# Optimization experiments

Hardware: AMD Instinct MI355X
Metric: run time of the kernel (lower is better)

Reference implementation:

```python
import jax, jax.numpy as jnp
import numpy as np

DN = ('NCHW', 'OIHW', 'NCHW')

def bn(x, g, b, m, v, eps=1e-5):
    # inference-mode BatchNorm2d over channel dim of NCHW
    s = g * jax.lax.rsqrt(v + eps)
    return x * s[:, None, None] + (b - m * s)[:, None, None]

def conv2d(x, w, pad):
    return jax.lax.conv_general_dilated(x, w, (1, 1), pad, dimension_numbers=DN)

def mamba(x, in_w, cw, cb, xp_w, dt_w, dt_b, A_log, Dp, out_w):
    # x: [B, L, d_model]
    B, L, dm = x.shape
    di = cw.shape[0]           # d_inner
    N = A_log.shape[1]         # d_state
    R = dt_w.shape[1]          # dt_rank
    K = cw.shape[2]            # d_conv
    xz = x @ in_w.T            # [B, L, 2*di]
    xi, z = xz[..., :di], xz[..., di:]
    # causal depthwise conv1d along L
    xc = jnp.transpose(xi, (0, 2, 1))  # [B, di, L]
    xc = jax.lax.conv_general_dilated(xc, cw, (1,), [(K - 1, 0)],
                                      dimension_numbers=('NCH', 'OIH', 'NCH'),
                                      feature_group_count=di)
    xc = jax.nn.silu(xc + cb[None, :, None])
    xc = jnp.transpose(xc, (0, 2, 1))  # [B, L, di]
    dbl = xc @ xp_w.T                  # [B, L, R+2N]
    dt, Bs, Cs = dbl[..., :R], dbl[..., R:R + N], dbl[..., R + N:]
    dt = jax.nn.softplus(dt @ dt_w.T + dt_b)        # [B, L, di]
    A = -jnp.exp(A_log)                              # [di, N]
    dA = jnp.exp(dt[..., None] * A)                  # [B, L, di, N]
    dBx = dt[..., None] * Bs[:, :, None, :] * xc[..., None]  # [B, L, di, N]

    def step(h, inp):
        a, bx, c = inp                               # [B,di,N],[B,di,N],[B,N]
        h = a * h + bx
        return h, jnp.einsum('bdn,bn->bd', h, c)

    h0 = jnp.zeros((B, di, N), x.dtype)
    _, ys = jax.lax.scan(step, h0, (jnp.transpose(dA, (1, 0, 2, 3)),
                                    jnp.transpose(dBx, (1, 0, 2, 3)),
                                    jnp.transpose(Cs, (1, 0, 2))))
    y = jnp.transpose(ys, (1, 0, 2)) + xc * Dp       # skip via D
    y = y * jax.nn.silu(z)                           # gate
    return y @ out_w.T                               # [B, L, dm]

def fwd(x, w1, g1, b1, m1, v1, w2, g2, b2, m2, v2,
        in_w, cw, cb, xp_w, dt_w, dt_b, A_log, Dp, out_w,
        w3, g3, b3, m3, v3, w4, g4, b4, m4, v4):
    x = jax.nn.gelu(bn(conv2d(x, w1, [(1, 1), (1, 1)]), g1, b1, m1, v1), approximate=False)
    x = jax.nn.silu(bn(conv2d(x, w2, [(0, 0), (0, 0)]), g2, b2, m2, v2))
    Bsz, Dc, H, W = x.shape
    t = jnp.transpose(x, (0, 2, 3, 1)).reshape(Bsz, H * W, Dc)
    t = mamba(t, in_w, cw, cb, xp_w, dt_w, dt_b, A_log, Dp, out_w)
    x = jnp.transpose(t.reshape(Bsz, H, W, Dc), (0, 3, 1, 2))
    x = jax.nn.silu(bn(conv2d(x, w3, [(0, 0), (0, 0)]), g3, b3, m3, v3))
    x = jax.nn.gelu(bn(conv2d(x, w4, [(1, 1), (1, 1)]), g4, b4, m4, v4), approximate=False)
    return x

def setup_inputs() -> dict:
    INC, D, OUTC = 96, 192, 192
    DI, N, R, K = 2 * D, 16, 12, 4   # d_inner, d_state, dt_rank, d_conv
    B, H, W = 8, 32, 32
    ks = jax.random.split(jax.random.key(0), 32)
    rn = lambda i, sh, s=0.05: s * jax.random.normal(ks[i], sh, dtype=jnp.float32)
    def bnp(i, c):
        k1, k2, k3, k4 = jax.random.split(ks[i], 4)
        return (1.0 + 0.1 * jax.random.normal(k1, (c,), dtype=jnp.float32),
                0.1 * jax.random.normal(k2, (c,), dtype=jnp.float32),
                0.1 * jax.random.normal(k3, (c,), dtype=jnp.float32),
                jax.random.uniform(k4, (c,), jnp.float32, 0.5, 1.5))
    g1, b1, m1, v1 = bnp(2, INC)
    g2, b2, m2, v2 = bnp(4, D)
    g3, b3, m3, v3 = bnp(6, OUTC)
    g4, b4, m4, v4 = bnp(8, OUTC)
    A_log = jnp.log(jnp.broadcast_to(jnp.arange(1, N + 1, dtype=jnp.float32), (DI, N)))
    return {
        'x': jax.random.normal(ks[0], (B, INC, H, W), dtype=jnp.float32),
        'w1': rn(1, (INC, INC, 3, 3)), 'g1': g1, 'b1': b1, 'm1': m1, 'v1': v1,
        'w2': rn(3, (D, INC, 1, 1)), 'g2': g2, 'b2': b2, 'm2': m2, 'v2': v2,
        'in_w': rn(10, (2 * DI, D), 0.02),
        'cw': rn(11, (DI, 1, K), 0.2),
        'cb': rn(12, (DI,), 0.02),
        'xp_w': rn(13, (R + 2 * N, DI), 0.05),
        'dt_w': rn(14, (DI, R), 0.1),
        'dt_b': rn(15, (DI,), 0.1) - 4.0,
        'A_log': A_log,
        'Dp': jnp.ones((DI,), dtype=jnp.float32),
        'out_w': rn(16, (D, DI), 0.05),
        'w3': rn(5, (OUTC, D, 1, 1)), 'g3': g3, 'b3': b3, 'm3': m3, 'v3': v3,
        'w4': rn(7, (OUTC, OUTC, 3, 3), 0.03), 'g4': g4, 'b4': b4, 'm4': m4, 'v4': v4,
    }

def reference(x, w1, g1, b1, m1, v1, w2, g2, b2, m2, v2,
              in_w, cw, cb, xp_w, dt_w, dt_b, A_log, Dp, out_w,
              w3, g3, b3, m3, v3, w4, g4, b4, m4, v4):
    return fwd(x, w1, g1, b1, m1, v1, w2, g2, b2, m2, v2,
               in_w, cw, cb, xp_w, dt_w, dt_b, A_log, Dp, out_w,
               w3, g3, b3, m3, v3, w4, g4, b4, m4, v4)
```

## Files before the change

### kernel.cpp

```cpp
#include <hip/hip_runtime.h>
#include <hip/hip_bf16.h>

using u16 = unsigned short;
using short8 = __attribute__((ext_vector_type(8))) short;
using f32x4  = __attribute__((ext_vector_type(4))) float;

constexpr int DI_ = 384;

constexpr size_t O_XZ   = 0;
constexpr size_t O_XCT  = O_XZ  + (size_t)8192*384;
constexpr size_t O_ZST  = O_XCT + (size_t)384*8192;
constexpr size_t O_DBLT = O_ZST + (size_t)384*8192;
constexpr size_t O_YFT  = O_DBLT+ (size_t)32*8192;
constexpr size_t O_B16  = O_YFT + (size_t)384*8192;
constexpr size_t O_DTT  = O_XZ;
constexpr size_t B_T1  = 0;
constexpr size_t B_T2  = B_T1  + (size_t)8192*96;
constexpr size_t B_XC  = B_T2  + (size_t)8192*192;
constexpr size_t B_XB1 = B_XC  + (size_t)8192*384;
constexpr size_t B_XB4 = B_XB1 + (size_t)8192*96;
constexpr size_t B_WT1 = B_XB4 + (size_t)8192*192;
constexpr size_t B_WT4 = B_WT1 + (size_t)9*96*96;
constexpr size_t B_INW = B_WT4 + (size_t)9*192*192;
constexpr size_t B_W2  = B_INW + (size_t)768*192;
constexpr size_t B_XP  = B_W2  + (size_t)192*96;
constexpr size_t B_WDT = B_XP  + (size_t)32*384;
constexpr size_t B_WOW = B_WDT + (size_t)384*384;

__device__ __forceinline__ u16 f2b(float f) {
    __hip_bfloat16 h = __float2bfloat16(f);
    return *reinterpret_cast<u16*>(&h);
}

struct PrepArgs {
    const float *w1, *w4, *in_w, *w2, *xp_w, *dt_w, *w3, *out_w, *x;
    u16 *wt1, *wt4, *inwb, *w2b, *xpb, *Wdt, *Wow, *Xb1;
};

__global__ __launch_bounds__(256) void prep_k(PrepArgs a) {
    const int job = blockIdx.y;
    const int stride = gridDim.x * 256;
    const int i0 = blockIdx.x * 256 + threadIdx.x;
    switch (job) {
    case 0:
        for (int i = i0; i < 9*96*96; i += stride) {
            int ci = i % 96, co = (i / 96) % 96, t = i / (96*96);
            a.wt1[i] = f2b(a.w1[((size_t)co*96 + ci)*9 + t]);
        } break;
    case 1:
        for (int i = i0; i < 9*192*192; i += stride) {
            int ci = i % 192, co = (i / 192) % 192, t = i / (192*192);
            a.wt4[i] = f2b(a.w4[((size_t)co*192 + ci)*9 + t]);
        } break;
    case 2:
        for (int i = i0; i < 768*192; i += stride) a.inwb[i] = f2b(a.in_w[i]);
        break;
    case 3:
        for (int i = i0; i < 192*96; i += stride) a.w2b[i] = f2b(a.w2[i]);
        break;
    case 4:
        for (int i = i0; i < 32*384; i += stride) {
            int r = i / 384, c = i % 384;
            a.xpb[i] = f2b(a.xp_w[(size_t)(12 + r)*384 + c]);
        } break;
    case 5:
        for (int i = i0; i < 384*384; i += stride) {
            int r = i / 384, c = i % 384;
            float s = 0.f;
            #pragma unroll
            for (int k = 0; k < 12; ++k) s += a.dt_w[r*12 + k] * a.xp_w[(size_t)k*384 + c];
            a.Wdt[i] = f2b(s);
        } break;
    case 6:
        for (int i = i0; i < 192*384; i += stride) {
            int o = i / 384, d = i % 384;
            float s = 0.f;
            for (int j = 0; j < 192; ++j) s += a.w3[(size_t)o*192 + j] * a.out_w[(size_t)j*384 + d];
            a.Wow[i] = f2b(s);
        } break;
    case 7:
        for (int i = i0; i < 8192*96; i += stride) {
            int ci = i % 96, px = i / 96;
            a.Xb1[i] = f2b(a.x[(((size_t)(px >> 10) * 96 + ci) << 10) | (size_t)(px & 1023)]);
        } break;
    }
}

template<int CIN, int COUT, int NTILE, int OUTM>
__global__ __launch_bounds__(256) void conv3x3_mfma_k(
    const u16* __restrict__ Xb, const u16* __restrict__ Wt,
    const float* __restrict__ g, const float* __restrict__ b,
    const float* __restrict__ m, const float* __restrict__ v,
    void* __restrict__ out)
{
    constexpr int LD = 40;
    constexpr int NT = NTILE / 16;
    __shared__ u16 As[4 * 36 * LD];
    __shared__ u16 Bs[9 * NTILE * LD];
    const int tid = threadIdx.x;
    const int wave = tid >> 6, lane = tid & 63;
    const int quad = lane >> 4, l16 = lane & 15;
    const int rowBase = blockIdx.x * 64;
    const int colBase = blockIdx.y * NTILE;
    const int img = rowBase >> 10;
    const int imgRow0 = (rowBase & 1023) >> 5;

    if (tid < 160) {
        int slot8 = tid / 20;
        int off = tid % 20;
        int hrow = slot8 >> 1;
        int hcol = (slot8 & 1) ? 33 : 0;
        ((unsigned*)As)[((hrow * 36 + hcol) * LD) / 2 + off] = 0u;
    }

    f32x4 acc[NT];
    #pragma unroll
    for (int nt = 0; nt < NT; ++nt)
        #pragma unroll
        for (int i = 0; i < 4; ++i) acc[nt][i] = 0.f;

    const int pxl = wave * 16 + l16;
    const int prow = pxl >> 5, pcol = pxl & 31;

    for (int ci0 = 0; ci0 < CIN; ci0 += 32) {
        __syncthreads();
        #pragma unroll
        for (int it = 0; it < 2; ++it) {
            int id = tid + it * 256;
            int pix = id >> 2, seg = id & 3;
            int hrow = pix >> 5, hcol = pix & 31;
            int grow = imgRow0 - 1 + hrow;
            uint4 va = make_uint4(0u, 0u, 0u, 0u);
            if ((unsigned)grow < 32u)
                va = *(const uint4*)(Xb +
                    (size_t)((img << 10) + (grow << 5) + hcol) * CIN + ci0 + seg * 8);
            *(uint4*)(As + (hrow * 36 + hcol + 1) * LD + seg * 8) = va;
        }
        constexpr int BT = 9 * NTILE * 4;
        for (int id = tid; id < BT; id += 256) {
            int t = id / (NTILE * 4);
            int r = (id >> 2) & (NTILE - 1);
            int seg = id & 3;
            uint4 vb = *(const uint4*)(Wt +
                ((size_t)t * COUT + colBase + r) * CIN + ci0 + seg * 8);
            *(uint4*)(Bs + (t * NTILE + r) * LD + seg * 8) = vb;
        }
        __syncthreads();
        #pragma unroll
        for (int t = 0; t < 9; ++t) {
            const int dr = t / 3 - 1, dc = t % 3 - 1;
            short8 a = *(const short8*)(As +
                ((prow + 1 + dr) * 36 + (pcol + 1 + dc)) * LD + quad * 8);
            #pragma unroll
            for (int nt = 0; nt < NT; ++nt) {
                short8 bf = *(const short8*)(Bs + (t * NTILE + nt * 16 + l16) * LD + quad * 8);
                acc[nt] = __builtin_amdgcn_mfma_f32_16x16x32_bf16(a, bf, acc[nt], 0, 0, 0);
            }
        }
    }

    const int px0 = rowBase + wave * 16 + quad * 4;
    #pragma unroll
    for (int nt = 0; nt < NT; ++nt) {
        const int co = colBase + nt * 16 + l16;
        const float sc = g[co] * rsqrtf(v[co] + 1e-5f);
        const float bb = b[co] - m[co] * sc;
        float o[4];
        #pragma unroll
        for (int r = 0; r < 4; ++r) {
            float xv = acc[nt][r] * sc + bb;
            o[r] = 0.5f * xv * (1.f + erff(xv * 0.70710678f));
        }
        if (OUTM == 2) {
            #pragma unroll
            for (int r = 0; r < 4; ++r)
                ((u16*)out)[(size_t)(px0 + r) * COUT + co] = f2b(o[r]);
        } else {
            const int oimg = px0 >> 10, off = px0 & 1023;
            *(float4*)((float*)out + (((size_t)oimg * COUT + co) << 10) + off) =
                make_float4(o[0], o[1], o[2], o[3]);
        }
    }
}

template<int NTILE, int EPI, int OUTM>
__device__ __forceinline__ void gemm_body(
    int M, int N, int K,
    const u16* __restrict__ Ab, const u16* __restrict__ Bb, void* __restrict__ C,
    const float* __restrict__ p0, const float* __restrict__ p1,
    const float* __restrict__ p2, const float* __restrict__ p3,
    int rowBase, int colBase, u16* As, u16* Bs)
{
    constexpr int LDA = 40;
    constexpr int NT = NTILE / 16;
    const int tid = threadIdx.x;
    const int wave = tid >> 6, lane = tid & 63;
    const int quad = lane >> 4, l16 = lane & 15;

    f32x4 acc[NT];
    #pragma unroll
    for (int nt = 0; nt < NT; ++nt)
        #pragma unroll
        for (int i = 0; i < 4; ++i) acc[nt][i] = 0.f;

    const int ar = tid >> 2, aseg = tid & 3;

    for (int k0 = 0; k0 < K; k0 += 32) {
        __syncthreads();
        uint4 va = *(const uint4*)(Ab + (size_t)(rowBase + ar) * K + k0 + aseg * 8);
        *(uint4*)(As + ar * LDA + aseg * 8) = va;
        if (tid < NTILE * 4) {
            int r = tid >> 2, seg = tid & 3;
            uint4 vb = *(const uint4*)(Bb + (size_t)(colBase + r) * K + k0 + seg * 8);
            *(uint4*)(Bs + r * LDA + seg * 8) = vb;
        }
        __syncthreads();
        short8 a = *(const short8*)(As + (wave * 16 + l16) * LDA + quad * 8);
        #pragma unroll
        for (int nt = 0; nt < NT; ++nt) {
            short8 bf = *(const short8*)(Bs + (nt * 16 + l16) * LDA + quad * 8);
            acc[nt] = __builtin_amdgcn_mfma_f32_16x16x32_bf16(a, bf, acc[nt], 0, 0, 0);
        }
    }

    const int px0 = rowBase + wave * 16 + quad * 4;
    #pragma unroll
    for (int nt = 0; nt < NT; ++nt) {
        const int co = colBase + nt * 16 + l16;
        float sc = 0.f, bb = 0.f;
        if (EPI == 1) {
            sc = p0[co] * rsqrtf(p3[co] + 1e-5f);
            bb = p1[co] - p2[co] * sc;
        } else if (EPI == 2) {
            bb = p0[co];
        }
        float o[4];
        #pragma unroll
        for (int r = 0; r < 4; ++r) {
            float xv = acc[nt][r];
            if (EPI == 1) {
                xv = xv * sc + bb;
                xv = xv / (1.f + __expf(-xv));
            } else if (EPI == 2) {
                xv += bb;
                xv = (xv > 20.f) ? xv : log1pf(__expf(xv));
            } else if (EPI == 3) {
                xv = xv / (1.f + __expf(-xv));
            }
            o[r] = xv;
        }
        if (OUTM == 3) {
            *(float4*)((float*)C + (size_t)co * M + px0) =
                make_float4(o[0], o[1], o[2], o[3]);
        } else if (OUTM == 2) {
            #pragma unroll
            for (int r = 0; r < 4; ++r)
                ((u16*)C)[(size_t)(px0 + r) * N + co] = f2b(o[r]);
        } else {
            #pragma unroll
            for (int r = 0; r < 4; ++r)
                ((float*)C)[(size_t)(px0 + r) * N + co] = o[r];
        }
    }
}

template<int NTILE, int EPI, int OUTM>
__global__ __launch_bounds__(256) void gemm_mfma_k(
    int M, int N, int K,
    const u16* __restrict__ Ab, const u16* __restrict__ Bb, void* __restrict__ C,
    const float* __restrict__ p0, const float* __restrict__ p1,
    const float* __restrict__ p2, const float* __restrict__ p3)
{
    __shared__ u16 As[64 * 40];
    __shared__ u16 Bs[NTILE * 40];
    gemm_body<NTILE, EPI, OUTM>(M, N, K, Ab, Bb, C, p0, p1, p2, p3,
                                blockIdx.x * 64, blockIdx.y * NTILE, As, Bs);
}

__global__ __launch_bounds__(256) void ip_k(
    const u16* __restrict__ t2b, const u16* __restrict__ inwb,
    float* __restrict__ xzb, float* __restrict__ zst)
{
    __shared__ u16 As[64 * 40];
    __shared__ u16 Bs[64 * 40];
    if (blockIdx.y < 6) {
        gemm_body<64, 0, 0>(8192, 384, 192, t2b, inwb, xzb,
                            nullptr, nullptr, nullptr, nullptr,
                            blockIdx.x * 64, blockIdx.y * 64, As, Bs);
    } else {
        gemm_body<64, 3, 3>(8192, 384, 192, t2b, inwb + (size_t)384*192, zst,
                            nullptr, nullptr, nullptr, nullptr,
                            blockIdx.x * 64, (blockIdx.y - 6) * 64, As, Bs);
    }
}

__global__ __launch_bounds__(256) void pd_k(
    const u16* __restrict__ xcb, const u16* __restrict__ Wdt,
    const u16* __restrict__ xpb, const float* __restrict__ dt_b,
    float* __restrict__ dtt, float* __restrict__ dblt)
{
    __shared__ u16 As[64 * 40];
    __shared__ u16 Bs[64 * 40];
    if (blockIdx.y < 6) {
        gemm_body<64, 2, 3>(8192, 384, 384, xcb, Wdt, dtt, dt_b, nullptr, nullptr, nullptr,
                            blockIdx.x * 64, blockIdx.y * 64, As, Bs);
    } else {
        gemm_body<32, 0, 3>(8192, 32, 384, xcb, xpb, dblt, nullptr, nullptr, nullptr, nullptr,
                            blockIdx.x * 64, 0, As, Bs);
    }
}

__global__ __launch_bounds__(256) void gemm_at_k(
    int M, int N, int K,
    const float* __restrict__ At, const u16* __restrict__ Bb, u16* __restrict__ C,
    const float* __restrict__ p0, const float* __restrict__ p1,
    const float* __restrict__ p2, const float* __restrict__ p3)
{
    constexpr int LDA = 40;
    constexpr int NTILE = 64, NT = 4;
    __shared__ u16 As[64 * LDA];
    __shared__ u16 Bs[NTILE * LDA];
    const int tid = threadIdx.x;
    const int wave = tid >> 6, lane = tid & 63;
    const int quad = lane >> 4, l16 = lane & 15;
    const int rowBase = blockIdx.x * 64;
    const int colBase = blockIdx.y * NTILE;

    f32x4 acc[NT];
    #pragma unroll
    for (int nt = 0; nt < NT; ++nt)
        #pragma unroll
        for (int i = 0; i < 4; ++i) acc[nt][i] = 0.f;

    const int krow = tid >> 3, mseg = tid & 7;

    for (int k0 = 0; k0 < K; k0 += 32) {
        __syncthreads();
        const float* src = At + (size_t)(k0 + krow) * M + rowBase + mseg * 4;
        float4 f0 = *(const float4*)(src);
        float4 f1 = *(const float4*)(src + 32);
        As[(mseg*4 + 0) * LDA + krow] = f2b(f0.x);
        As[(mseg*4 + 1) * LDA + krow] = f2b(f0.y);
        As[(mseg*4 + 2) * LDA + krow] = f2b(f0.z);
        As[(mseg*4 + 3) * LDA + krow] = f2b(f0.w);
        As[(mseg*4 + 32) * LDA + krow] = f2b(f1.x);
        As[(mseg*4 + 33) * LDA + krow] = f2b(f1.y);
        As[(mseg*4 + 34) * LDA + krow] = f2b(f1.z);
        As[(mseg*4 + 35) * LDA + krow] = f2b(f1.w);
        if (tid < NTILE * 4) {
            int r = tid >> 2, seg = tid & 3;
            uint4 vb = *(const uint4*)(Bb + (size_t)(colBase + r) * K + k0 + seg * 8);
            *(uint4*)(Bs + r * LDA + seg * 8) = vb;
        }
        __syncthreads();
        short8 a = *(const short8*)(As + (wave * 16 + l16) * LDA + quad * 8);
        #pragma unroll
        for (int nt = 0; nt < NT; ++nt) {
            short8 bf = *(const short8*)(Bs + (nt * 16 + l16) * LDA + quad * 8);
            acc[nt] = __builtin_amdgcn_mfma_f32_16x16x32_bf16(a, bf, acc[nt], 0, 0, 0);
        }
    }

    const int px0 = rowBase + wave * 16 + quad * 4;
    #pragma unroll
    for (int nt = 0; nt < NT; ++nt) {
        const int co = colBase + nt * 16 + l16;
        const float sc = p0[co] * rsqrtf(p3[co] + 1e-5f);
        const float bb = p1[co] - p2[co] * sc;
        #pragma unroll
        for (int r = 0; r < 4; ++r) {
            float xv = acc[nt][r] * sc + bb;
            xv = xv / (1.f + __expf(-xv));
            C[(size_t)(px0 + r) * N + co] = f2b(xv);
        }
    }
}

__global__ __launch_bounds__(256) void dwconv_k(
    const float* __restrict__ xz, const float* __restrict__ cw, const float* __restrict__ cb,
    u16* __restrict__ xcb, float* __restrict__ xct)
{
    __shared__ float T[64][65];
    const int tid = threadIdx.x;
    const int cl = tid & 63, rq = tid >> 6;
    const int mBase = blockIdx.x * 64, cBase = blockIdx.y * 64;
    const int c = cBase + cl;
    const float w0 = cw[c*4+0], w1 = cw[c*4+1], w2 = cw[c*4+2], w3 = cw[c*4+3];
    const float bias = cb[c];
    #pragma unroll
    for (int rr = 0; rr < 16; ++rr) {
        int ml = rr * 4 + rq;
        int bl = mBase + ml;
        int l = bl & 1023;
        float acc = bias + xz[(size_t)bl * 384 + c] * w3;
        if (l >= 1) acc += xz[(size_t)(bl-1) * 384 + c] * w2;
        if (l >= 2) acc += xz[(size_t)(bl-2) * 384 + c] * w1;
        if (l >= 3) acc += xz[(size_t)(bl-3) * 384 + c] * w0;
        float s = acc / (1.f + __expf(-acc));
        xcb[(size_t)bl * DI_ + c] = f2b(s);
        T[ml][cl] = s;
    }
    __syncthreads();
    #pragma unroll
    for (int rr = 0; rr < 16; ++rr) {
        int dl = rr * 4 + rq;
        xct[(size_t)(cBase + dl) * 8192 + mBase + cl] = T[cl][dl];
    }
}

__global__ __launch_bounds__(256) void scan_k(
    const float* __restrict__ dtt, const float* __restrict__ dblt,
    const float* __restrict__ xct, const float* __restrict__ zst,
    const float* __restrict__ A_log, const float* __restrict__ Dp,
    float* __restrict__ yft)
{
    const int bd = blockIdx.x;
    const int b = bd / DI_, d = bd % DI_;
    const int tid = threadIdx.x;
    const size_t tb = (size_t)d * 8192 + (size_t)b * 1024;
    const size_t nb = (size_t)b * 1024;
    const int t4 = tid * 4;

    __shared__ float LH[16][257];
    __shared__ float SD[257];
    __shared__ float SH[16][17];
    __shared__ float SP[16][17];
    __shared__ float SSD[17];
    __shared__ float AndS[16];

    const float4 dt4 = *(const float4*)(dtt + tb + t4);
    const float4 xc4 = *(const float4*)(xct + tb + t4);
    const float dtxc[4] = {dt4.x*xc4.x, dt4.y*xc4.y, dt4.z*xc4.z, dt4.w*xc4.w};

    float And[16];
    #pragma unroll
    for (int n = 0; n < 16; ++n) And[n] = -__expf(A_log[d*16 + n]);
    if (tid < 16) AndS[tid] = -__expf(A_log[d*16 + tid]);
    SD[tid] = dt4.x + dt4.y + dt4.z + dt4.w;

    #pragma unroll
    for (int n = 0; n < 16; ++n) {
        const float4 bs4 = *(const float4*)(dblt + (size_t)n * 8192 + nb + t4);
        float h = dtxc[0] * bs4.x;
        h = __expf(dt4.y * And[n]) * h + dtxc[1] * bs4.y;
        h = __expf(dt4.z * And[n]) * h + dtxc[2] * bs4.z;
        h = __expf(dt4.w * And[n]) * h + dtxc[3] * bs4.w;
        LH[n][tid] = h;
    }
    __syncthreads();

    {
        const int n = tid & 15, s = tid >> 4;
        const float An = AndS[n];
        float H = 0.f, ssd = 0.f;
        #pragma unroll
        for (int k = 0; k < 16; ++k) {
            const int c = s * 16 + k;
            float sd = SD[c];
            H = __expf(An * sd) * H + LH[n][c];
            ssd += sd;
        }
        SH[n][s] = H;
        if (n == 0) SSD[s] = ssd;
    }
    __syncthreads();

    if (tid < 16) {
        const float An = AndS[tid];
        float Hp = 0.f;
        #pragma unroll
        for (int s = 0; s < 16; ++s) {
            SP[tid][s] = Hp;
            Hp = __expf(An * SSD[s]) * Hp + SH[tid][s];
        }
    }
    __syncthreads();

    {
        const int n = tid & 15, s = tid >> 4;
        const float An = AndS[n];
        float st = SP[n][s];
        #pragma unroll
        for (int k = 0; k < 16; ++k) {
            const int c = s * 16 + k;
            float a = __expf(An * SD[c]);
            float h = LH[n][c];
            LH[n][c] = st;
            st = a * st + h;
        }
    }
    __syncthreads();

    float y0 = 0.f, y1 = 0.f, y2 = 0.f, y3 = 0.f;
    #pragma unroll
    for (int n = 0; n < 16; ++n) {
        float h = LH[n][tid];
        const float4 bs4 = *(const float4*)(dblt + (size_t)n * 8192 + nb + t4);
        const float4 cs4 = *(const float4*)(dblt + (size_t)(16 + n) * 8192 + nb + t4);
        h = __expf(dt4.x * And[n]) * h + dtxc[0]*bs4.x; y0 += h * cs4.x;
        h = __expf(dt4.y * And[n]) * h + dtxc[1]*bs4.y; y1 += h * cs4.y;
        h = __expf(dt4.z * And[n]) * h + dtxc[2]*bs4.z; y2 += h * cs4.z;
        h = __expf(dt4.w * And[n]) * h + dtxc[3]*bs4.w; y3 += h * cs4.w;
    }
    const float dp = Dp[d];
    const float4 zs4 = *(const float4*)(zst + tb + t4);
    float4 o;
    o.x = (y0 + xc4.x * dp) * zs4.x;
    o.y = (y1 + xc4.y * dp) * zs4.y;
    o.z = (y2 + xc4.z * dp) * zs4.z;
    o.w = (y3 + xc4.w * dp) * zs4.w;
    *(float4*)(yft + tb + t4) = o;
}

extern "C" void kernel_launch(void* const* d_in, const int* in_sizes, int n_in,
                              void* d_out, int out_size, void* d_ws, size_t ws_size,
                              hipStream_t stream) {
    const float* x     = (const float*)d_in[0];
    const float* w1    = (const float*)d_in[1];
    const float* g1    = (const float*)d_in[2];
    const float* b1    = (const float*)d_in[3];
    const float* m1    = (const float*)d_in[4];
    const float* v1    = (const float*)d_in[5];
    const float* w2    = (const float*)d_in[6];
    const float* g2    = (const float*)d_in[7];
    const float* b2    = (const float*)d_in[8];
    const float* m2    = (const float*)d_in[9];
    const float* v2    = (const float*)d_in[10];
    const float* in_w  = (const float*)d_in[11];
    const float* cw    = (const float*)d_in[12];
    const float* cb    = (const float*)d_in[13];
    const float* xp_w  = (const float*)d_in[14];
    const float* dt_w  = (const float*)d_in[15];
    const float* dt_b  = (const float*)d_in[16];
    const float* A_log = (const float*)d_in[17];
    const float* Dp    = (const float*)d_in[18];
    const float* out_w = (const float*)d_in[19];
    const float* w3    = (const float*)d_in[20];
    const float* g3    = (const float*)d_in[21];
    const float* b3    = (const float*)d_in[22];
    const float* m3    = (const float*)d_in[23];
    const float* v3    = (const float*)d_in[24];
    const float* w4    = (const float*)d_in[25];
    const float* g4    = (const float*)d_in[26];
    const float* b4    = (const float*)d_in[27];
    const float* m4    = (const float*)d_in[28];
    const float* v4    = (const float*)d_in[29];

    float* ws   = (float*)d_ws;
    float* xzb  = ws + O_XZ;
    float* xct  = ws + O_XCT;
    float* zst  = ws + O_ZST;
    float* dblt = ws + O_DBLT;
    float* yft  = ws + O_YFT;
    float* dtt  = ws + O_DTT;
    u16* b16  = (u16*)(ws + O_B16);
    u16* t1b  = b16 + B_T1;
    u16* t2b  = b16 + B_T2;
    u16* xcb  = b16 + B_XC;
    u16* Xb1  = b16 + B_XB1;
    u16* Xb4  = b16 + B_XB4;
    u16* wt1  = b16 + B_WT1;
    u16* wt4  = b16 + B_WT4;
    u16* inwb = b16 + B_INW;
    u16* w2b  = b16 + B_W2;
    u16* xpb  = b16 + B_XP;
    u16* Wdt  = b16 + B_WDT;
    u16* Wow  = b16 + B_WOW;

    PrepArgs pa;
    pa.w1 = w1; pa.w4 = w4; pa.in_w = in_w; pa.w2 = w2; pa.xp_w = xp_w;
    pa.dt_w = dt_w; pa.w3 = w3; pa.out_w = out_w; pa.x = x;
    pa.wt1 = wt1; pa.wt4 = wt4; pa.inwb = inwb; pa.w2b = w2b; pa.xpb = xpb;
    pa.Wdt = Wdt; pa.Wow = Wow; pa.Xb1 = Xb1;
    prep_k<<<dim3(256, 8), 256, 0, stream>>>(pa);

    conv3x3_mfma_k<96, 96, 32, 2><<<dim3(128, 3), 256, 0, stream>>>(
        Xb1, wt1, g1, b1, m1, v1, t1b);

    gemm_mfma_k<64, 1, 2><<<dim3(128, 3), 256, 0, stream>>>(
        8192, 192, 96, t1b, w2b, t2b, g2, b2, m2, v2);

    ip_k<<<dim3(128, 12), 256, 0, stream>>>(t2b, inwb, xzb, zst);

    dwconv_k<<<dim3(128, 6), 256, 0, stream>>>(xzb, cw, cb, xcb, xct);

    pd_k<<<dim3(128, 7), 256, 0, stream>>>(xcb, Wdt, xpb, dt_b, dtt, dblt);

    scan_k<<<8 * DI_, 256, 0, stream>>>(dtt, dblt, xct, zst, A_log, Dp, yft);

    gemm_at_k<<<dim3(128, 3), 256, 0, stream>>>(
        8192, 192, 384, yft, Wow, Xb4, g3, b3, m3, v3);

    conv3x3_mfma_k<192, 192, 64, 1><<<dim3(128, 3), 256, 0, stream>>>(
        Xb4, wt4, g4, b4, m4, v4, (float*)d_out);
}
```

Before: 264.7 us.

## Store Mamba intermediates in bf16, stage conv output through LDS, retile final conv

The in-projection now writes xz and the gated z buffer as bf16 instead of fp32. The depthwise conv and scan kernels read these bf16 values and the transposed conv output as bf16, which halves the memory traffic for these intermediates. The final conv's NCHW fp32 epilogue now transposes through shared memory so each store is a coalesced float4 row. Its column tile is halved from 64 to 32, doubling the grid to add parallelism. The bf16 storage lowers the precision of the xz, z and xc values used in the scan.

```diff
diff --git a/kernel.cpp b/kernel.cpp
--- a/kernel.cpp
+++ b/kernel.cpp
@@ -31,6 +31,11 @@
     __hip_bfloat16 h = __float2bfloat16(f);
     return *reinterpret_cast<u16*>(&h);
 }
+__device__ __forceinline__ float b2f(u16 u) {
+    return __uint_as_float(((unsigned)u) << 16);
+}
+__device__ __forceinline__ float b2f_lo(unsigned u) { return __uint_as_float(u << 16); }
+__device__ __forceinline__ float b2f_hi(unsigned u) { return __uint_as_float(u & 0xffff0000u); }
 
 struct PrepArgs {
     const float *w1, *w4, *in_w, *w2, *xp_w, *dt_w, *w3, *out_w, *x;
@@ -160,25 +165,42 @@
     }
 
     const int px0 = rowBase + wave * 16 + quad * 4;
-    #pragma unroll
-    for (int nt = 0; nt < NT; ++nt) {
-        const int co = colBase + nt * 16 + l16;
-        const float sc = g[co] * rsqrtf(v[co] + 1e-5f);
-        const float bb = b[co] - m[co] * sc;
-        float o[4];
-        #pragma unroll
-        for (int r = 0; r < 4; ++r) {
-            float xv = acc[nt][r] * sc + bb;
-            o[r] = 0.5f * xv * (1.f + erff(xv * 0.70710678f));
-        }
-        if (OUTM == 2) {
+    if (OUTM == 2) {
+        #pragma unroll
+        for (int nt = 0; nt < NT; ++nt) {
+            const int co = colBase + nt * 16 + l16;
+            const float sc = g[co] * rsqrtf(v[co] + 1e-5f);
+            const float bb = b[co] - m[co] * sc;
             #pragma unroll
-            for (int r = 0; r < 4; ++r)
-                ((u16*)out)[(size_t)(px0 + r) * COUT + co] = f2b(o[r]);
-        } else {
-            const int oimg = px0 >> 10, off = px0 & 1023;
-            *(float4*)((float*)out + (((size_t)oimg * COUT + co) << 10) + off) =
-                make_float4(o[0], o[1], o[2], o[3]);
+            for (int r = 0; r < 4; ++r) {
+                float xv = acc[nt][r] * sc + bb;
+                float gel = 0.5f * xv * (1.f + erff(xv * 0.70710678f));
+                ((u16*)out)[(size_t)(px0 + r) * COUT + co] = f2b(gel);
+            }
+        }
+    } else {
+        float* Tout = (float*)As;
+        const int pxl0 = wave * 16 + quad * 4;
+        __syncthreads();
+        #pragma unroll
+        for (int nt = 0; nt < NT; ++nt) {
+            const int co = colBase + nt * 16 + l16;
+            const float sc = g[co] * rsqrtf(v[co] + 1e-5f);
+            const float bb = b[co] - m[co] * sc;
+            #pragma unroll
+            for (int r = 0; r < 4; ++r) {
+                float xv = acc[nt][r] * sc + bb;
+                Tout[(nt * 16 + l16) * 68 + pxl0 + r] =
+                    0.5f * xv * (1.f + erff(xv * 0.70710678f));
+            }
+        }
+        __syncthreads();
+        const int off0 = rowBase & 1023;
+        for (int s = tid; s < NTILE * 16; s += 256) {
+            int co = s >> 4, p4 = s & 15;
+            float4 vv = *(const float4*)(Tout + co * 68 + p4 * 4);
+            *(float4*)((float*)out + (((size_t)img * COUT + colBase + co) << 10)
+                       + off0 + p4 * 4) = vv;
         }
     }
 }
@@ -252,6 +274,11 @@
         if (OUTM == 3) {
             *(float4*)((float*)C + (size_t)co * M + px0) =
                 make_float4(o[0], o[1], o[2], o[3]);
+        } else if (OUTM == 4) {
+            uint2 pk;
+            pk.x = (unsigned)f2b(o[0]) | ((unsigned)f2b(o[1]) << 16);
+            pk.y = (unsigned)f2b(o[2]) | ((unsigned)f2b(o[3]) << 16);
+            *(uint2*)((u16*)C + (size_t)co * M + px0) = pk;
         } else if (OUTM == 2) {
             #pragma unroll
             for (int r = 0; r < 4; ++r)
@@ -279,16 +306,16 @@
 
 __global__ __launch_bounds__(256) void ip_k(
     const u16* __restrict__ t2b, const u16* __restrict__ inwb,
-    float* __restrict__ xzb, float* __restrict__ zst)
+    u16* __restrict__ xzb16, u16* __restrict__ zst16)
 {
     __shared__ u16 As[64 * 40];
     __shared__ u16 Bs[64 * 40];
     if (blockIdx.y < 6) {
-        gemm_body<64, 0, 0>(8192, 384, 192, t2b, inwb, xzb,
+        gemm_body<64, 0, 2>(8192, 384, 192, t2b, inwb, xzb16,
                             nullptr, nullptr, nullptr, nullptr,
                             blockIdx.x * 64, blockIdx.y * 64, As, Bs);
     } else {
-        gemm_body<64, 3, 3>(8192, 384, 192, t2b, inwb + (size_t)384*192, zst,
+        gemm_body<64, 3, 4>(8192, 384, 192, t2b, inwb + (size_t)384*192, zst16,
                             nullptr, nullptr, nullptr, nullptr,
                             blockIdx.x * 64, (blockIdx.y - 6) * 64, As, Bs);
     }
@@ -377,8 +404,8 @@
 }
 
 __global__ __launch_bounds__(256) void dwconv_k(
-    const float* __restrict__ xz, const float* __restrict__ cw, const float* __restrict__ cb,
-    u16* __restrict__ xcb, float* __restrict__ xct)
+    const u16* __restrict__ xz16, const float* __restrict__ cw, const float* __restrict__ cb,
+    u16* __restrict__ xcb, u16* __restrict__ xct16)
 {
     __shared__ float T[64][65];
     const int tid = threadIdx.x;
@@ -392,10 +419,10 @@
         int ml = rr * 4 + rq;
         int bl = mBase + ml;
         int l = bl & 1023;
-        float acc = bias + xz[(size_t)bl * 384 + c] * w3;
-        if (l >= 1) acc += xz[(size_t)(bl-1) * 384 + c] * w2;
-        if (l >= 2) acc += xz[(size_t)(bl-2) * 384 + c] * w1;
-        if (l >= 3) acc += xz[(size_t)(bl-3) * 384 + c] * w0;
+        float acc = bias + b2f(xz16[(size_t)bl * 384 + c]) * w3;
+        if (l >= 1) acc += b2f(xz16[(size_t)(bl-1) * 384 + c]) * w2;
+        if (l >= 2) acc += b2f(xz16[(size_t)(bl-2) * 384 + c]) * w1;
+        if (l >= 3) acc += b2f(xz16[(size_t)(bl-3) * 384 + c]) * w0;
         float s = acc / (1.f + __expf(-acc));
         xcb[(size_t)bl * DI_ + c] = f2b(s);
         T[ml][cl] = s;
@@ -404,13 +431,13 @@
     #pragma unroll
     for (int rr = 0; rr < 16; ++rr) {
         int dl = rr * 4 + rq;
-        xct[(size_t)(cBase + dl) * 8192 + mBase + cl] = T[cl][dl];
+        xct16[(size_t)(cBase + dl) * 8192 + mBase + cl] = f2b(T[cl][dl]);
     }
 }
 
 __global__ __launch_bounds__(256) void scan_k(
     const float* __restrict__ dtt, const float* __restrict__ dblt,
-    const float* __restrict__ xct, const float* __restrict__ zst,
+    const u16* __restrict__ xct16, const u16* __restrict__ zst16,
     const float* __restrict__ A_log, const float* __restrict__ Dp,
     float* __restrict__ yft)
 {
@@ -429,8 +456,10 @@
     __shared__ float AndS[16];
 
     const float4 dt4 = *(const float4*)(dtt + tb + t4);
-    const float4 xc4 = *(const float4*)(xct + tb + t4);
-    const float dtxc[4] = {dt4.x*xc4.x, dt4.y*xc4.y, dt4.z*xc4.z, dt4.w*xc4.w};
+    const uint2 xcu = *(const uint2*)(xct16 + tb + t4);
+    const float xc0 = b2f_lo(xcu.x), xc1 = b2f_hi(xcu.x);
+    const float xc2 = b2f_lo(xcu.y), xc3 = b2f_hi(xcu.y);
+    const float dtxc[4] = {dt4.x*xc0, dt4.y*xc1, dt4.z*xc2, dt4.w*xc3};
 
     float And[16];
     #pragma unroll
@@ -503,12 +532,12 @@
         h = __expf(dt4.w * And[n]) * h + dtxc[3]*bs4.w; y3 += h * cs4.w;
     }
     const float dp = Dp[d];
-    const float4 zs4 = *(const float4*)(zst + tb + t4);
+    const uint2 zsu = *(const uint2*)(zst16 + tb + t4);
     float4 o;
-    o.x = (y0 + xc4.x * dp) * zs4.x;
-    o.y = (y1 + xc4.y * dp) * zs4.y;
-    o.z = (y2 + xc4.z * dp) * zs4.z;
-    o.w = (y3 + xc4.w * dp) * zs4.w;
+    o.x = (y0 + xc0 * dp) * b2f_lo(zsu.x);
+    o.y = (y1 + xc1 * dp) * b2f_hi(zsu.x);
+    o.z = (y2 + xc2 * dp) * b2f_lo(zsu.y);
+    o.w = (y3 + xc3 * dp) * b2f_hi(zsu.y);
     *(float4*)(yft + tb + t4) = o;
 }
 
@@ -547,9 +576,9 @@
     const float* v4    = (const float*)d_in[29];
 
     float* ws   = (float*)d_ws;
-    float* xzb  = ws + O_XZ;
-    float* xct  = ws + O_XCT;
-    float* zst  = ws + O_ZST;
+    u16*   xzb16 = (u16*)(ws + O_XZ);
+    u16*   xct16 = (u16*)(ws + O_XCT);
+    u16*   zst16 = (u16*)(ws + O_ZST);
     float* dblt = ws + O_DBLT;
     float* yft  = ws + O_YFT;
     float* dtt  = ws + O_DTT;
@@ -580,17 +609,17 @@
     gemm_mfma_k<64, 1, 2><<<dim3(128, 3), 256, 0, stream>>>(
         8192, 192, 96, t1b, w2b, t2b, g2, b2, m2, v2);
 
-    ip_k<<<dim3(128, 12), 256, 0, stream>>>(t2b, inwb, xzb, zst);
-
-    dwconv_k<<<dim3(128, 6), 256, 0, stream>>>(xzb, cw, cb, xcb, xct);
+    ip_k<<<dim3(128, 12), 256, 0, stream>>>(t2b, inwb, xzb16, zst16);
+
+    dwconv_k<<<dim3(128, 6), 256, 0, stream>>>(xzb16, cw, cb, xcb, xct16);
 
     pd_k<<<dim3(128, 7), 256, 0, stream>>>(xcb, Wdt, xpb, dt_b, dtt, dblt);
 
-    scan_k<<<8 * DI_, 256, 0, stream>>>(dtt, dblt, xct, zst, A_log, Dp, yft);
+    scan_k<<<8 * DI_, 256, 0, stream>>>(dtt, dblt, xct16, zst16, A_log, Dp, yft);
 
     gemm_at_k<<<dim3(128, 3), 256, 0, stream>>>(
         8192, 192, 384, yft, Wow, Xb4, g3, b3, m3, v3);
 
-    conv3x3_mfma_k<192, 192, 64, 1><<<dim3(128, 3), 256, 0, stream>>>(
+    conv3x3_mfma_k<192, 192, 32, 1><<<dim3(128, 6), 256, 0, stream>>>(
         Xb4, wt4, g4, b4, m4, v4, (float*)d_out);
 }
```

Result: faster. 250.4 us (-5.4%).
